# Kernel optimization log

Measured on AMD Instinct MI355X. Metric: run time of the kernel, lower is better.

The kernel has to match this reference:

```python
import jax, jax.numpy as jnp
import numpy as np

STRIDE = 1
PADDING = 1

def setup_inputs() -> dict:
    key = jax.random.key(0)
    k1, k2 = jax.random.split(key)
    x = jax.random.normal(k1, (16, 64, 224, 224), dtype=jnp.float32)
    weight = jax.random.normal(k2, (64, 64, 3, 3), dtype=jnp.float32)
    return {"x": x, "weight": weight}

def reference(x, weight):
    # Module's per-tap shift-and-add loop is exactly cross-correlation conv2d:
    # weight indexed [out, in, kh, kw] with ZeroPad2d(padding) and given stride.
    return jax.lax.conv_general_dilated(
        x, weight,
        window_strides=(STRIDE, STRIDE),
        padding=((PADDING, PADDING), (PADDING, PADDING)),
        dimension_numbers=("NCHW", "OIHW", "NCHW"),
    )
```

## Files before the change

### kernel.cpp

```cpp
#include <hip/hip_runtime.h>
#include <stdint.h>


#define HH 224
#define WW 224
#define CHW (HH * WW)
#define PLANE 4352
#define NSLOT 18
#define XT_ROWB 28928
#define XT_NB   6537728
#define WB_BYTES 73728
#define WS_NEED (WB_BYTES + 16 * (size_t)XT_NB)

typedef short bf16x8 __attribute__((ext_vector_type(8)));
typedef float f32x16 __attribute__((ext_vector_type(16)));
typedef __attribute__((address_space(1))) const char GCHAR;
typedef __attribute__((address_space(3))) char LCHAR;

__device__ __forceinline__ unsigned short f2bf(float f) {
    union { float f; unsigned int u; } v; v.f = f;
    unsigned int u = v.u;
    return (unsigned short)((u + 0x7fffu + ((u >> 16) & 1u)) >> 16);
}

#define SGB  __builtin_amdgcn_sched_group_barrier
#define MFMA __builtin_amdgcn_mfma_f32_32x32x16_bf16

__device__ __forceinline__ void block_fence_lds() {
    asm volatile("s_waitcnt lgkmcnt(0)" ::: "memory");
    __builtin_amdgcn_s_barrier();
    __builtin_amdgcn_sched_barrier(0);
}

__global__ void wprep_kernel(const float* __restrict__ wgt, unsigned short* __restrict__ wb) {
    const int i = blockIdx.x * 256 + threadIdx.x;
    if (i >= 36864) return;
    const int j   = i & 7;
    const int oc  = (i >> 3) & 63;
    const int g   = (i >> 9) & 1;
    const int ks  = i >> 10;
    const int tap = ks >> 2;
    const int c   = (ks & 3) * 16 + g * 8 + j;
    wb[i] = f2bf(wgt[(oc * 64 + c) * 9 + tap]);
}

__global__ __launch_bounds__(256)
void xprep_kernel(const float* __restrict__ x, unsigned short* __restrict__ xt) {
    __shared__ __align__(16) unsigned short tile[226 * 64];
    const int tid = threadIdx.x;
    const int b   = blockIdx.x;
    const int n   = b / 226;
    const int hp  = b % 226;
    bf16x8* orow = (bf16x8*)((char*)xt + (size_t)(n * 226 + hp) * XT_ROWB);

    if (hp == 0 || hp == 225) {
        const bf16x8 z = {};
        for (int i = tid; i < 1808; i += 256) orow[i] = z;
        return;
    }
    if (tid < 64) { tile[tid] = 0; tile[225 * 64 + tid] = 0; }

    const float* xr = x + (size_t)n * 64 * CHW + (size_t)(hp - 1) * WW;
    for (int i = tid; i < 64 * 56; i += 256) {
        const int c  = i / 56;
        const int w4 = i % 56;
        const float4 v = *(const float4*)(xr + (size_t)c * CHW + w4 * 4);
        const int wp0 = w4 * 4 + 1;
        const int cb  = c * 2;
        *(unsigned short*)((char*)tile + (wp0    ) * 128 + (cb ^ ((((wp0    ) >> 2) & 7) << 4))) = f2bf(v.x);
        *(unsigned short*)((char*)tile + (wp0 + 1) * 128 + (cb ^ ((((wp0 + 1) >> 2) & 7) << 4))) = f2bf(v.y);
        *(unsigned short*)((char*)tile + (wp0 + 2) * 128 + (cb ^ ((((wp0 + 2) >> 2) & 7) << 4))) = f2bf(v.z);
        *(unsigned short*)((char*)tile + (wp0 + 3) * 128 + (cb ^ ((((wp0 + 3) >> 2) & 7) << 4))) = f2bf(v.w);
    }
    __syncthreads();
    for (int i = tid; i < 1808; i += 256) {
        const int wp = i >> 3, k = i & 7;
        orow[i] = ((const bf16x8*)tile)[wp * 8 + (k ^ ((wp >> 2) & 7))];
    }
}

#define MMA_CQ(dw, cq, WFU) do {                                              \
    const int off_ = (((cq) * 32 + g16) ^ swz_);                              \
    const bf16x8 B0 = *(const bf16x8*)(ldsB + sl0 + wb_ + off_);              \
    const bf16x8 B1 = *(const bf16x8*)(ldsB + sl1 + wb_ + off_);              \
    const bf16x8 B2 = *(const bf16x8*)(ldsB + sl2 + wb_ + off_);              \
    const bf16x8 B3 = *(const bf16x8*)(ldsB + sl3 + wb_ + off_);              \
    const bf16x8 B4 = *(const bf16x8*)(ldsB + sl4 + wb_ + off_);              \
    const bf16x8 B5 = *(const bf16x8*)(ldsB + sl5 + wb_ + off_);              \
    a0 = MFMA(wfrag[(dw)*4 + (cq)], B0, a0, 0, 0, 0);                         \
    a1 = MFMA(wfrag[(dw)*4 + (cq)], B1, a1, 0, 0, 0);                         \
    a2 = MFMA(wfrag[(dw)*4 + (cq)], B2, a2, 0, 0, 0);                         \
    a3 = MFMA(wfrag[(dw)*4 + (cq)], B3, a3, 0, 0, 0);                         \
    a0 = MFMA(wfrag[12 + (dw)*4 + (cq)], B1, a0, 0, 0, 0);                    \
    a1 = MFMA(wfrag[12 + (dw)*4 + (cq)], B2, a1, 0, 0, 0);                    \
    a2 = MFMA(wfrag[12 + (dw)*4 + (cq)], B3, a2, 0, 0, 0);                    \
    a3 = MFMA(wfrag[12 + (dw)*4 + (cq)], B4, a3, 0, 0, 0);                    \
    a0 = MFMA(WFU, B2, a0, 0, 0, 0);                                          \
    a1 = MFMA(WFU, B3, a1, 0, 0, 0);                                          \
    a2 = MFMA(WFU, B4, a2, 0, 0, 0);                                          \
    a3 = MFMA(WFU, B5, a3, 0, 0, 0);                                          \
    SGB(0x100, 6, 0); SGB(0x008, 12, 0);                                      \
} while (0)

#define SECTION(dw, cqp, WFU0, WFU1, WFLD0, WFLD1, ldw, lcqp) do {            \
    WFLD0 = *(const bf16x8*)(wlane + ((6 + (ldw))*4 + 2*(lcqp)    ) * 1024);  \
    WFLD1 = *(const bf16x8*)(wlane + ((6 + (ldw))*4 + 2*(lcqp) + 1) * 1024);  \
    const int wl_  = s + (dw);                                                \
    const int swz_ = (wl_ & 7) << 4;                                          \
    const int wb_  = wl_ * 128;                                               \
    MMA_CQ(dw, 2*(cqp),     WFU0);                                            \
    MMA_CQ(dw, 2*(cqp) + 1, WFU1);                                            \
} while (0)

#define GLOAD_ROW(r) do {                                                     \
    const char* seg_ = xtn + (size_t)((r) + 1) * XT_ROWB;                     \
    char* lp_ = ldsB + (((r) + NSLOT) % NSLOT) * PLANE;                       \
    _Pragma("unroll")                                                         \
    for (int p_ = 0; p_ < 4; ++p_)                                            \
        __builtin_amdgcn_global_load_lds((GCHAR*)(seg_ + p_ * 1024 + lconst), \
                                         (LCHAR*)(lp_ + p_ * 1024), 16, 0, 0);\
    if (lane < 16)                                                            \
        __builtin_amdgcn_global_load_lds((GCHAR*)(seg_ + 4096 + lconst),      \
                                         (LCHAR*)(lp_ + 4096), 16, 0, 0);     \
} while (0)

__global__ __launch_bounds__(256, 2)
void conv3x3_gl(const unsigned short* __restrict__ xt, const unsigned short* __restrict__ wb,
                float* __restrict__ out) {
    __shared__ __align__(16) unsigned short lds[NSLOT * 34 * 64];
    char* ldsB = (char*)lds;

    const int tid  = threadIdx.x;
    const int lane = tid & 63;
    const int wv   = tid >> 6;
    const int och  = wv & 1;
    const int rg4  = wv >> 1;
    const int s    = lane & 31;
    const int g    = lane >> 5;
    const int g16  = g * 16;

    const int bid = blockIdx.x;
    const int n   = bid / 28;
    const int rem = bid % 28;
    const int ws  = rem / 4;
    const int hc  = rem % 4;
    const int wbase = ws * 32;
    const int h0    = hc * 56;

    const int lconst = ((lane >> 3) << 7) + (((lane & 7) ^ (lane >> 3)) << 4);
    const char* xtn = (const char*)xt + (size_t)n * XT_NB + (size_t)wbase * 128;

    const unsigned short* wlane = wb + g * 512 + (och * 32 + s) * 8;
    bf16x8 wfrag[24];
#pragma unroll
    for (int ks = 0; ks < 24; ++ks)
        wfrag[ks] = *(const bf16x8*)(wlane + ks * 1024);
    bf16x8 wfA0 = *(const bf16x8*)(wlane + 24 * 1024);
    bf16x8 wfA1 = *(const bf16x8*)(wlane + 25 * 1024);
    bf16x8 wfB0 = {}, wfB1 = {};

    for (int rr = 0; rr < 10; ++rr) {
        const int r = h0 - 1 + rr;
        const char* seg = xtn + (size_t)(r + 1) * XT_ROWB;
        char* lp = ldsB + ((r + NSLOT) % NSLOT) * PLANE;
        __builtin_amdgcn_global_load_lds((GCHAR*)(seg + wv * 1024 + lconst),
                                         (LCHAR*)(lp + wv * 1024), 16, 0, 0);
        if (wv == 0 && lane < 16)
            __builtin_amdgcn_global_load_lds((GCHAR*)(seg + 4096 + lconst),
                                             (LCHAR*)(lp + 4096), 16, 0, 0);
    }
    __syncthreads();

#pragma unroll 1
    for (int it = 0; it < 7; ++it) {
        const int h  = h0 + 8 * it;
        const int hb = h + 4 * rg4;

        if (it < 6) {
            const int r0 = h + 9 + 2 * wv;
            GLOAD_ROW(r0);
            GLOAD_ROW(r0 + 1);
        }

        int t_ = (hb - 1 + NSLOT) % NSLOT;
        const int sl0 = t_ * PLANE; t_ = (t_ + 1 == NSLOT) ? 0 : t_ + 1;
        const int sl1 = t_ * PLANE; t_ = (t_ + 1 == NSLOT) ? 0 : t_ + 1;
        const int sl2 = t_ * PLANE; t_ = (t_ + 1 == NSLOT) ? 0 : t_ + 1;
        const int sl3 = t_ * PLANE; t_ = (t_ + 1 == NSLOT) ? 0 : t_ + 1;
        const int sl4 = t_ * PLANE; t_ = (t_ + 1 == NSLOT) ? 0 : t_ + 1;
        const int sl5 = t_ * PLANE;

        f32x16 a0 = {}, a1 = {}, a2 = {}, a3 = {};

        SECTION(0, 0, wfA0, wfA1, wfB0, wfB1, 0, 1);
        SECTION(0, 1, wfB0, wfB1, wfA0, wfA1, 1, 0);
        SECTION(1, 0, wfA0, wfA1, wfB0, wfB1, 1, 1);
        SECTION(1, 1, wfB0, wfB1, wfA0, wfA1, 2, 0);
        SECTION(2, 0, wfA0, wfA1, wfB0, wfB1, 2, 1);
        SECTION(2, 1, wfB0, wfB1, wfA0, wfA1, 0, 0);

        float* po = out + (n * 64 + och * 32 + 4 * g) * CHW + hb * WW + wbase + s;
#pragma unroll
        for (int rg = 0; rg < 16; ++rg) {
            const int o_ = ((rg & 3) + 8 * (rg >> 2)) * CHW;
            po[o_]          = a0[rg];
            po[o_ + WW]     = a1[rg];
            po[o_ + 2 * WW] = a2[rg];
            po[o_ + 3 * WW] = a3[rg];
        }

        __syncthreads();
    }
}

#define STI(k) do { if (st) {                                                 \
    const int r_ = h + 9 + (k);                                               \
    const bool ok_ = (r_ < HH);                                               \
    _Pragma("unroll")                                                         \
    for (int j = 0; j < 8; ++j) pv[j] = ok_ ? pxm[j*CHW + r_*WW] : 0.f;       \
    if (tid >= 240) {                                                         \
        const bool okh_ = ok_ && hokw;                                        \
        _Pragma("unroll")                                                     \
        for (int j = 0; j < 8; ++j) hv[j] = okh_ ? pxh[j*CHW + r_*WW] : 0.f;  \
    } } } while (0)

#define STW(k) do { if (st) {                                                 \
    int sw_ = slw + (k); if (sw_ >= NSLOT) sw_ -= NSLOT;                      \
    bf16x8 f_;                                                                \
    _Pragma("unroll")                                                         \
    for (int j = 0; j < 8; ++j) f_[j] = (short)f2bf(pv[j]);                   \
    *(bf16x8*)(ldsB + sw_ * PLANE + lom) = f_;                                \
    if (tid >= 240) {                                                         \
        bf16x8 fh_;                                                           \
        _Pragma("unroll")                                                     \
        for (int j = 0; j < 8; ++j) fh_[j] = (short)f2bf(hv[j]);              \
        *(bf16x8*)(ldsB + sw_ * PLANE + loh) = fh_;                           \
    } } } while (0)

__global__ __launch_bounds__(256, 2)
void conv3x3_fb(const float* __restrict__ x, const unsigned short* __restrict__ wb,
                float* __restrict__ out) {
    __shared__ __align__(16) unsigned short lds[NSLOT * 34 * 64];
    char* ldsB = (char*)lds;

    const int tid  = threadIdx.x;
    const int lane = tid & 63;
    const int wv   = tid >> 6;
    const int och  = wv & 1;
    const int rg4  = wv >> 1;
    const int s    = lane & 31;
    const int g    = lane >> 5;
    const int g16  = g * 16;

    const int bid = blockIdx.x;
    const int n   = bid / 28;
    const int rem = bid % 28;
    const int ws  = rem / 4;
    const int hc  = rem % 4;
    const int wbase = ws * 32;
    const int h0    = hc * 56;

    const unsigned short* wlane = wb + g * 512 + (och * 32 + s) * 8;
    bf16x8 wfrag[24];
#pragma unroll
    for (int ks = 0; ks < 24; ++ks)
        wfrag[ks] = *(const bf16x8*)(wlane + ks * 1024);
    bf16x8 wfA0 = *(const bf16x8*)(wlane + 24 * 1024);
    bf16x8 wfA1 = *(const bf16x8*)(wlane + 25 * 1024);
    bf16x8 wfB0 = {}, wfB1 = {};

    for (int p = tid; p < 10 * 272; p += 256) {
        const int rrel = p / 272;
        const int q  = p % 272;
        const int c8 = q / 34;
        const int wl = q % 34;
        const int r  = h0 - 1 + rrel;
        const int gw = wbase - 1 + wl;
        bf16x8 f = {};
        if (r >= 0 && r < HH && gw >= 0 && gw < WW) {
            const float* px = x + (n * 64 + c8 * 8) * CHW + r * WW + gw;
#pragma unroll
            for (int j = 0; j < 8; ++j) f[j] = (short)f2bf(px[j * CHW]);
        }
        *(bf16x8*)(ldsB + ((r + NSLOT) % NSLOT) * PLANE + wl * 128
                   + ((c8 * 16) ^ ((wl & 7) << 4))) = f;
    }

    const int c8m = tid >> 5;
    const int wlm = 1 + (tid & 31);
    const float* pxm = x + (n * 64 + c8m * 8) * CHW + (wbase + (tid & 31));
    const int lom = wlm * 128 + ((c8m * 16) ^ ((wlm & 7) << 4));
    const int c8h = lane & 7;
    const int wlh = ((lane >> 3) & 1) * 33;
    const int gwh = wbase - 1 + wlh;
    const bool hokw = (gwh >= 0 && gwh < WW);
    const float* pxh = x + (n * 64 + c8h * 8) * CHW + gwh;
    const int loh = wlh * 128 + ((c8h * 16) ^ ((wlh & 7) << 4));

    block_fence_lds();

#pragma unroll 1
    for (int it = 0; it < 7; ++it) {
        const int h  = h0 + 8 * it;
        const int hb = h + 4 * rg4;
        const bool st = (it < 6);
        const int slw = (h + 9) % NSLOT;

        int t_ = (hb - 1 + NSLOT) % NSLOT;
        const int sl0 = t_ * PLANE; t_ = (t_ + 1 == NSLOT) ? 0 : t_ + 1;
        const int sl1 = t_ * PLANE; t_ = (t_ + 1 == NSLOT) ? 0 : t_ + 1;
        const int sl2 = t_ * PLANE; t_ = (t_ + 1 == NSLOT) ? 0 : t_ + 1;
        const int sl3 = t_ * PLANE; t_ = (t_ + 1 == NSLOT) ? 0 : t_ + 1;
        const int sl4 = t_ * PLANE; t_ = (t_ + 1 == NSLOT) ? 0 : t_ + 1;
        const int sl5 = t_ * PLANE;

        float pv[8], hv[8];
        f32x16 a0 = {}, a1 = {}, a2 = {}, a3 = {};

        STI(0); SECTION(0, 0, wfA0, wfA1, wfB0, wfB1, 0, 1); STW(0);
        STI(1); SECTION(0, 1, wfB0, wfB1, wfA0, wfA1, 1, 0); STW(1);
        STI(2); SECTION(1, 0, wfA0, wfA1, wfB0, wfB1, 1, 1); STW(2);
        STI(3); SECTION(1, 1, wfB0, wfB1, wfA0, wfA1, 2, 0); STW(3);
        STI(4); SECTION(2, 0, wfA0, wfA1, wfB0, wfB1, 2, 1); STW(4);
        STI(5); SECTION(2, 1, wfB0, wfB1, wfA0, wfA1, 0, 0); STW(5);

        float* po = out + (n * 64 + och * 32 + 4 * g) * CHW + hb * WW + wbase + s;
        STI(6);
#pragma unroll
        for (int rg = 0; rg < 16; ++rg) {
            const int o_ = ((rg & 3) + 8 * (rg >> 2)) * CHW;
            po[o_]      = a0[rg];
            po[o_ + WW] = a1[rg];
        }
        STW(6); STI(7);
#pragma unroll
        for (int rg = 0; rg < 16; ++rg) {
            const int o_ = ((rg & 3) + 8 * (rg >> 2)) * CHW;
            po[o_ + 2 * WW] = a2[rg];
            po[o_ + 3 * WW] = a3[rg];
        }
        STW(7);

        block_fence_lds();
    }
}

extern "C" void kernel_launch(void* const* d_in, const int* in_sizes, int n_in,
                              void* d_out, int out_size, void* d_ws, size_t ws_size,
                              hipStream_t stream) {
    const float* x   = (const float*)d_in[0];
    const float* wgt = (const float*)d_in[1];
    float* out       = (float*)d_out;
    unsigned short* wbuf = (unsigned short*)d_ws;

    wprep_kernel<<<dim3(144), dim3(256), 0, stream>>>(wgt, wbuf);
    if (ws_size >= WS_NEED) {
        unsigned short* xt = (unsigned short*)((char*)d_ws + WB_BYTES);
        xprep_kernel<<<dim3(16 * 226), dim3(256), 0, stream>>>(x, xt);
        conv3x3_gl<<<dim3(448), dim3(256), 0, stream>>>(xt, wbuf, out);
    } else {
        conv3x3_fb<<<dim3(448), dim3(256), 0, stream>>>(x, wbuf, out);
    }
}
```

Before: 161.6 us.

## Shrink conv tile to 2 rows per wave for higher occupancy and more blocks

Rewrites the main bf16 MFMA conv kernel so each wave computes 2 output rows instead of 4. The launch grows to 896 blocks of 28 rows each, and the LDS ring shrinks from 18 to 10 row slots. Only the first kw tap's weight fragments stay resident in registers; the other two taps' fragments stream from global memory each step. Launch bounds rise to 3 blocks per CU, aiming for better latency hiding and load balance across CUs. The costs are reloading the streamed weight fragments every iteration and reusing fewer input rows per LDS load.

```diff
diff --git a/kernel.cpp b/kernel.cpp
--- a/kernel.cpp
+++ b/kernel.cpp
@@ -7,6 +7,7 @@
 #define CHW (HH * WW)
 #define PLANE 4352
 #define NSLOT 18
+#define NSLOTG 10
 #define XT_ROWB 28928
 #define XT_NB   6537728
 #define WB_BYTES 73728
@@ -76,6 +77,112 @@
     for (int i = tid; i < 1808; i += 256) {
         const int wp = i >> 3, k = i & 7;
         orow[i] = ((const bf16x8*)tile)[wp * 8 + (k ^ ((wp >> 2) & 7))];
+    }
+}
+
+#define GLOAD_ROW(r) do {                                                     \
+    const char* seg_ = xtn + (size_t)((r) + 1) * XT_ROWB;                     \
+    char* lp_ = ldsB + (((r) + NSLOTG) % NSLOTG) * PLANE;                     \
+    _Pragma("unroll")                                                         \
+    for (int p_ = 0; p_ < 4; ++p_)                                            \
+        __builtin_amdgcn_global_load_lds((GCHAR*)(seg_ + p_ * 1024 + lconst), \
+                                         (LCHAR*)(lp_ + p_ * 1024), 16, 0, 0);\
+    if (lane < 16)                                                            \
+        __builtin_amdgcn_global_load_lds((GCHAR*)(seg_ + 4096 + lconst),      \
+                                         (LCHAR*)(lp_ + 4096), 16, 0, 0);     \
+} while (0)
+
+#define STEP(j, U1_, U2_) do {                                                \
+    const int wl_  = s + ((j) >> 2);                                          \
+    const int off_ = wl_ * 128 + ((((j) & 3) * 32 + g16) ^ ((wl_ & 7) << 4)); \
+    const bf16x8 B0 = *(const bf16x8*)(ldsB + sl0 + off_);                    \
+    const bf16x8 B1 = *(const bf16x8*)(ldsB + sl1 + off_);                    \
+    const bf16x8 B2 = *(const bf16x8*)(ldsB + sl2 + off_);                    \
+    const bf16x8 B3 = *(const bf16x8*)(ldsB + sl3 + off_);                    \
+    a0 = MFMA(wfrag[(j)], B0, a0, 0, 0, 0);                                   \
+    a1 = MFMA(wfrag[(j)], B1, a1, 0, 0, 0);                                   \
+    a0 = MFMA(U1_, B1, a0, 0, 0, 0);                                          \
+    a1 = MFMA(U1_, B2, a1, 0, 0, 0);                                          \
+    a0 = MFMA(U2_, B2, a0, 0, 0, 0);                                          \
+    a1 = MFMA(U2_, B3, a1, 0, 0, 0);                                          \
+    SGB(0x100, 4, 0); SGB(0x008, 6, 0);                                       \
+    U1_ = *(const bf16x8*)(wlane + (12 + ((j) + 4) % 12) * 1024);             \
+    U2_ = *(const bf16x8*)(wlane + (24 + ((j) + 4) % 12) * 1024);             \
+} while (0)
+
+__global__ __launch_bounds__(256, 3)
+void conv3x3_gl(const unsigned short* __restrict__ xt, const unsigned short* __restrict__ wb,
+                float* __restrict__ out) {
+    __shared__ __align__(16) unsigned short lds[NSLOTG * 34 * 64];
+    char* ldsB = (char*)lds;
+
+    const int tid  = threadIdx.x;
+    const int lane = tid & 63;
+    const int wv   = tid >> 6;
+    const int och  = wv & 1;
+    const int rp   = wv >> 1;
+    const int s    = lane & 31;
+    const int g    = lane >> 5;
+    const int g16  = g * 16;
+
+    const int bid = blockIdx.x;
+    const int n   = bid / 56;
+    const int rem = bid % 56;
+    const int ws  = rem / 8;
+    const int hc  = rem % 8;
+    const int wbase = ws * 32;
+    const int h0    = hc * 28;
+
+    const int lconst = ((lane >> 3) << 7) + (((lane & 7) ^ (lane >> 3)) << 4);
+    const char* xtn = (const char*)xt + (size_t)n * XT_NB + (size_t)wbase * 128;
+
+    const unsigned short* wlane = wb + g * 512 + (och * 32 + s) * 8;
+    bf16x8 wfrag[12];
+#pragma unroll
+    for (int ks = 0; ks < 12; ++ks)
+        wfrag[ks] = *(const bf16x8*)(wlane + ks * 1024);
+    bf16x8 Q1a = *(const bf16x8*)(wlane + 12 * 1024);
+    bf16x8 Q1b = *(const bf16x8*)(wlane + 13 * 1024);
+    bf16x8 Q1c = *(const bf16x8*)(wlane + 14 * 1024);
+    bf16x8 Q1d = *(const bf16x8*)(wlane + 15 * 1024);
+    bf16x8 Q2a = *(const bf16x8*)(wlane + 24 * 1024);
+    bf16x8 Q2b = *(const bf16x8*)(wlane + 25 * 1024);
+    bf16x8 Q2c = *(const bf16x8*)(wlane + 26 * 1024);
+    bf16x8 Q2d = *(const bf16x8*)(wlane + 27 * 1024);
+
+    for (int rr = wv; rr < 6; rr += 4) {
+        const int r = h0 - 1 + rr;
+        GLOAD_ROW(r);
+    }
+    __syncthreads();
+
+#pragma unroll 1
+    for (int it = 0; it < 7; ++it) {
+        const int h  = h0 + 4 * it;
+        const int hb = h + 2 * rp;
+
+        if (it < 6) GLOAD_ROW(h + 5 + wv);
+
+        const int sl0 = ((hb - 1 + 2 * NSLOTG) % NSLOTG) * PLANE;
+        const int sl1 = ((hb     + 2 * NSLOTG) % NSLOTG) * PLANE;
+        const int sl2 = ((hb + 1) % NSLOTG) * PLANE;
+        const int sl3 = ((hb + 2) % NSLOTG) * PLANE;
+
+        f32x16 a0 = {}, a1 = {};
+
+        STEP(0, Q1a, Q2a); STEP(1, Q1b, Q2b); STEP(2, Q1c, Q2c); STEP(3, Q1d, Q2d);
+        STEP(4, Q1a, Q2a); STEP(5, Q1b, Q2b); STEP(6, Q1c, Q2c); STEP(7, Q1d, Q2d);
+        STEP(8, Q1a, Q2a); STEP(9, Q1b, Q2b); STEP(10, Q1c, Q2c); STEP(11, Q1d, Q2d);
+
+        float* po = out + (n * 64 + och * 32 + 4 * g) * CHW + hb * WW + wbase + s;
+#pragma unroll
+        for (int rg = 0; rg < 16; ++rg) {
+            const int o_ = ((rg & 3) + 8 * (rg >> 2)) * CHW;
+            po[o_]      = a0[rg];
+            po[o_ + WW] = a1[rg];
+        }
+
+        __syncthreads();
     }
 }
 
@@ -112,107 +219,6 @@
     MMA_CQ(dw, 2*(cqp) + 1, WFU1);                                            \
 } while (0)
 
-#define GLOAD_ROW(r) do {                                                     \
-    const char* seg_ = xtn + (size_t)((r) + 1) * XT_ROWB;                     \
-    char* lp_ = ldsB + (((r) + NSLOT) % NSLOT) * PLANE;                       \
-    _Pragma("unroll")                                                         \
-    for (int p_ = 0; p_ < 4; ++p_)                                            \
-        __builtin_amdgcn_global_load_lds((GCHAR*)(seg_ + p_ * 1024 + lconst), \
-                                         (LCHAR*)(lp_ + p_ * 1024), 16, 0, 0);\
-    if (lane < 16)                                                            \
-        __builtin_amdgcn_global_load_lds((GCHAR*)(seg_ + 4096 + lconst),      \
-                                         (LCHAR*)(lp_ + 4096), 16, 0, 0);     \
-} while (0)
-
-__global__ __launch_bounds__(256, 2)
-void conv3x3_gl(const unsigned short* __restrict__ xt, const unsigned short* __restrict__ wb,
-                float* __restrict__ out) {
-    __shared__ __align__(16) unsigned short lds[NSLOT * 34 * 64];
-    char* ldsB = (char*)lds;
-
-    const int tid  = threadIdx.x;
-    const int lane = tid & 63;
-    const int wv   = tid >> 6;
-    const int och  = wv & 1;
-    const int rg4  = wv >> 1;
-    const int s    = lane & 31;
-    const int g    = lane >> 5;
-    const int g16  = g * 16;
-
-    const int bid = blockIdx.x;
-    const int n   = bid / 28;
-    const int rem = bid % 28;
-    const int ws  = rem / 4;
-    const int hc  = rem % 4;
-    const int wbase = ws * 32;
-    const int h0    = hc * 56;
-
-    const int lconst = ((lane >> 3) << 7) + (((lane & 7) ^ (lane >> 3)) << 4);
-    const char* xtn = (const char*)xt + (size_t)n * XT_NB + (size_t)wbase * 128;
-
-    const unsigned short* wlane = wb + g * 512 + (och * 32 + s) * 8;
-    bf16x8 wfrag[24];
-#pragma unroll
-    for (int ks = 0; ks < 24; ++ks)
-        wfrag[ks] = *(const bf16x8*)(wlane + ks * 1024);
-    bf16x8 wfA0 = *(const bf16x8*)(wlane + 24 * 1024);
-    bf16x8 wfA1 = *(const bf16x8*)(wlane + 25 * 1024);
-    bf16x8 wfB0 = {}, wfB1 = {};
-
-    for (int rr = 0; rr < 10; ++rr) {
-        const int r = h0 - 1 + rr;
-        const char* seg = xtn + (size_t)(r + 1) * XT_ROWB;
-        char* lp = ldsB + ((r + NSLOT) % NSLOT) * PLANE;
-        __builtin_amdgcn_global_load_lds((GCHAR*)(seg + wv * 1024 + lconst),
-                                         (LCHAR*)(lp + wv * 1024), 16, 0, 0);
-        if (wv == 0 && lane < 16)
-            __builtin_amdgcn_global_load_lds((GCHAR*)(seg + 4096 + lconst),
-                                             (LCHAR*)(lp + 4096), 16, 0, 0);
-    }
-    __syncthreads();
-
-#pragma unroll 1
-    for (int it = 0; it < 7; ++it) {
-        const int h  = h0 + 8 * it;
-        const int hb = h + 4 * rg4;
-
-        if (it < 6) {
-            const int r0 = h + 9 + 2 * wv;
-            GLOAD_ROW(r0);
-            GLOAD_ROW(r0 + 1);
-        }
-
-        int t_ = (hb - 1 + NSLOT) % NSLOT;
-        const int sl0 = t_ * PLANE; t_ = (t_ + 1 == NSLOT) ? 0 : t_ + 1;
-        const int sl1 = t_ * PLANE; t_ = (t_ + 1 == NSLOT) ? 0 : t_ + 1;
-        const int sl2 = t_ * PLANE; t_ = (t_ + 1 == NSLOT) ? 0 : t_ + 1;
-        const int sl3 = t_ * PLANE; t_ = (t_ + 1 == NSLOT) ? 0 : t_ + 1;
-        const int sl4 = t_ * PLANE; t_ = (t_ + 1 == NSLOT) ? 0 : t_ + 1;
-        const int sl5 = t_ * PLANE;
-
-        f32x16 a0 = {}, a1 = {}, a2 = {}, a3 = {};
-
-        SECTION(0, 0, wfA0, wfA1, wfB0, wfB1, 0, 1);
-        SECTION(0, 1, wfB0, wfB1, wfA0, wfA1, 1, 0);
-        SECTION(1, 0, wfA0, wfA1, wfB0, wfB1, 1, 1);
-        SECTION(1, 1, wfB0, wfB1, wfA0, wfA1, 2, 0);
-        SECTION(2, 0, wfA0, wfA1, wfB0, wfB1, 2, 1);
-        SECTION(2, 1, wfB0, wfB1, wfA0, wfA1, 0, 0);
-
-        float* po = out + (n * 64 + och * 32 + 4 * g) * CHW + hb * WW + wbase + s;
-#pragma unroll
-        for (int rg = 0; rg < 16; ++rg) {
-            const int o_ = ((rg & 3) + 8 * (rg >> 2)) * CHW;
-            po[o_]          = a0[rg];
-            po[o_ + WW]     = a1[rg];
-            po[o_ + 2 * WW] = a2[rg];
-            po[o_ + 3 * WW] = a3[rg];
-        }
-
-        __syncthreads();
-    }
-}
-
 #define STI(k) do { if (st) {                                                 \
     const int r_ = h + 9 + (k);                                               \
     const bool ok_ = (r_ < HH);                                               \
@@ -357,7 +363,7 @@
     if (ws_size >= WS_NEED) {
         unsigned short* xt = (unsigned short*)((char*)d_ws + WB_BYTES);
         xprep_kernel<<<dim3(16 * 226), dim3(256), 0, stream>>>(x, xt);
-        conv3x3_gl<<<dim3(448), dim3(256), 0, stream>>>(xt, wbuf, out);
+        conv3x3_gl<<<dim3(16 * 7 * 8), dim3(256), 0, stream>>>(xt, wbuf, out);
     } else {
         conv3x3_fb<<<dim3(448), dim3(256), 0, stream>>>(x, wbuf, out);
     }
```

After: 211.1 us. 1.31x slower.

## Retile width to 28 columns so grid has 512 blocks filling all CUs

Applied to the files above, without the earlier changes.

Changes the fast-path conv kernel tiling from 32-wide to 28-wide column strips. This gives 8 strips per image and a grid of 512 blocks instead of 448, which should spread the work more evenly over the 256 CUs with 2 blocks each and avoid a partial second wave. The LDS plane shrinks to 30 columns (plus padding), and loads are adjusted to match. Each MFMA still computes 32 columns, so 4 of 32 lanes' outputs are discarded (about 12.5% wasted compute). The fallback kernel keeps the old plane size through separate macros.

```diff
diff --git a/kernel.cpp b/kernel.cpp
--- a/kernel.cpp
+++ b/kernel.cpp
@@ -5,7 +5,7 @@
 #define HH 224
 #define WW 224
 #define CHW (HH * WW)
-#define PLANE 4352
+#define PLANE 3840
 #define NSLOT 18
 #define XT_ROWB 28928
 #define XT_NB   6537728
@@ -116,18 +116,18 @@
     const char* seg_ = xtn + (size_t)((r) + 1) * XT_ROWB;                     \
     char* lp_ = ldsB + (((r) + NSLOT) % NSLOT) * PLANE;                       \
     _Pragma("unroll")                                                         \
-    for (int p_ = 0; p_ < 4; ++p_)                                            \
+    for (int p_ = 0; p_ < 3; ++p_)                                            \
         __builtin_amdgcn_global_load_lds((GCHAR*)(seg_ + p_ * 1024 + lconst), \
                                          (LCHAR*)(lp_ + p_ * 1024), 16, 0, 0);\
-    if (lane < 16)                                                            \
-        __builtin_amdgcn_global_load_lds((GCHAR*)(seg_ + 4096 + lconst),      \
-                                         (LCHAR*)(lp_ + 4096), 16, 0, 0);     \
+    if (lane < 48)                                                            \
+        __builtin_amdgcn_global_load_lds((GCHAR*)(seg_ + 3072 + lconst),      \
+                                         (LCHAR*)(lp_ + 3072), 16, 0, 0);     \
 } while (0)
 
 __global__ __launch_bounds__(256, 2)
 void conv3x3_gl(const unsigned short* __restrict__ xt, const unsigned short* __restrict__ wb,
                 float* __restrict__ out) {
-    __shared__ __align__(16) unsigned short lds[NSLOT * 34 * 64];
+    __shared__ __align__(16) unsigned short lds[NSLOT * 30 * 64 + 256];
     char* ldsB = (char*)lds;
 
     const int tid  = threadIdx.x;
@@ -140,11 +140,11 @@
     const int g16  = g * 16;
 
     const int bid = blockIdx.x;
-    const int n   = bid / 28;
-    const int rem = bid % 28;
+    const int n   = bid / 32;
+    const int rem = bid % 32;
     const int ws  = rem / 4;
     const int hc  = rem % 4;
-    const int wbase = ws * 32;
+    const int wbase = ws * 28;
     const int h0    = hc * 56;
 
     const int lconst = ((lane >> 3) << 7) + (((lane & 7) ^ (lane >> 3)) << 4);
@@ -163,11 +163,9 @@
         const int r = h0 - 1 + rr;
         const char* seg = xtn + (size_t)(r + 1) * XT_ROWB;
         char* lp = ldsB + ((r + NSLOT) % NSLOT) * PLANE;
-        __builtin_amdgcn_global_load_lds((GCHAR*)(seg + wv * 1024 + lconst),
-                                         (LCHAR*)(lp + wv * 1024), 16, 0, 0);
-        if (wv == 0 && lane < 16)
-            __builtin_amdgcn_global_load_lds((GCHAR*)(seg + 4096 + lconst),
-                                             (LCHAR*)(lp + 4096), 16, 0, 0);
+        if (wv < 3 || lane < 48)
+            __builtin_amdgcn_global_load_lds((GCHAR*)(seg + wv * 1024 + lconst),
+                                             (LCHAR*)(lp + wv * 1024), 16, 0, 0);
     }
     __syncthreads();
 
@@ -199,20 +197,23 @@
         SECTION(2, 0, wfA0, wfA1, wfB0, wfB1, 2, 1);
         SECTION(2, 1, wfB0, wfB1, wfA0, wfA1, 0, 0);
 
-        float* po = out + (n * 64 + och * 32 + 4 * g) * CHW + hb * WW + wbase + s;
-#pragma unroll
-        for (int rg = 0; rg < 16; ++rg) {
-            const int o_ = ((rg & 3) + 8 * (rg >> 2)) * CHW;
-            po[o_]          = a0[rg];
-            po[o_ + WW]     = a1[rg];
-            po[o_ + 2 * WW] = a2[rg];
-            po[o_ + 3 * WW] = a3[rg];
+        if (s < 28) {
+            float* po = out + (n * 64 + och * 32 + 4 * g) * CHW + hb * WW + wbase + s;
+#pragma unroll
+            for (int rg = 0; rg < 16; ++rg) {
+                const int o_ = ((rg & 3) + 8 * (rg >> 2)) * CHW;
+                po[o_]          = a0[rg];
+                po[o_ + WW]     = a1[rg];
+                po[o_ + 2 * WW] = a2[rg];
+                po[o_ + 3 * WW] = a3[rg];
+            }
         }
 
         __syncthreads();
     }
 }
 
+#define PLANE_FB 4352
 #define STI(k) do { if (st) {                                                 \
     const int r_ = h + 9 + (k);                                               \
     const bool ok_ = (r_ < HH);                                               \
@@ -229,13 +230,46 @@
     bf16x8 f_;                                                                \
     _Pragma("unroll")                                                         \
     for (int j = 0; j < 8; ++j) f_[j] = (short)f2bf(pv[j]);                   \
-    *(bf16x8*)(ldsB + sw_ * PLANE + lom) = f_;                                \
+    *(bf16x8*)(ldsB + sw_ * PLANE_FB + lom) = f_;                             \
     if (tid >= 240) {                                                         \
         bf16x8 fh_;                                                           \
         _Pragma("unroll")                                                     \
         for (int j = 0; j < 8; ++j) fh_[j] = (short)f2bf(hv[j]);              \
-        *(bf16x8*)(ldsB + sw_ * PLANE + loh) = fh_;                           \
+        *(bf16x8*)(ldsB + sw_ * PLANE_FB + loh) = fh_;                        \
     } } } while (0)
+
+#define MMA_CQ_FB(dw, cq, WFU) do {                                           \
+    const int off_ = (((cq) * 32 + g16) ^ swz_);                              \
+    const bf16x8 B0 = *(const bf16x8*)(ldsB + sl0 + wb_ + off_);              \
+    const bf16x8 B1 = *(const bf16x8*)(ldsB + sl1 + wb_ + off_);              \
+    const bf16x8 B2 = *(const bf16x8*)(ldsB + sl2 + wb_ + off_);              \
+    const bf16x8 B3 = *(const bf16x8*)(ldsB + sl3 + wb_ + off_);              \
+    const bf16x8 B4 = *(const bf16x8*)(ldsB + sl4 + wb_ + off_);              \
+    const bf16x8 B5 = *(const bf16x8*)(ldsB + sl5 + wb_ + off_);              \
+    a0 = MFMA(wfrag[(dw)*4 + (cq)], B0, a0, 0, 0, 0);                         \
+    a1 = MFMA(wfrag[(dw)*4 + (cq)], B1, a1, 0, 0, 0);                         \
+    a2 = MFMA(wfrag[(dw)*4 + (cq)], B2, a2, 0, 0, 0);                         \
+    a3 = MFMA(wfrag[(dw)*4 + (cq)], B3, a3, 0, 0, 0);                         \
+    a0 = MFMA(wfrag[12 + (dw)*4 + (cq)], B1, a0, 0, 0, 0);                    \
+    a1 = MFMA(wfrag[12 + (dw)*4 + (cq)], B2, a1, 0, 0, 0);                    \
+    a2 = MFMA(wfrag[12 + (dw)*4 + (cq)], B3, a2, 0, 0, 0);                    \
+    a3 = MFMA(wfrag[12 + (dw)*4 + (cq)], B4, a3, 0, 0, 0);                    \
+    a0 = MFMA(WFU, B2, a0, 0, 0, 0);                                          \
+    a1 = MFMA(WFU, B3, a1, 0, 0, 0);                                          \
+    a2 = MFMA(WFU, B4, a2, 0, 0, 0);                                          \
+    a3 = MFMA(WFU, B5, a3, 0, 0, 0);                                          \
+    SGB(0x100, 6, 0); SGB(0x008, 12, 0);                                      \
+} while (0)
+
+#define SECTION_FB(dw, cqp, WFU0, WFU1, WFLD0, WFLD1, ldw, lcqp) do {         \
+    WFLD0 = *(const bf16x8*)(wlane + ((6 + (ldw))*4 + 2*(lcqp)    ) * 1024);  \
+    WFLD1 = *(const bf16x8*)(wlane + ((6 + (ldw))*4 + 2*(lcqp) + 1) * 1024);  \
+    const int wl_  = s + (dw);                                                \
+    const int swz_ = (wl_ & 7) << 4;                                          \
+    const int wb_  = wl_ * 128;                                               \
+    MMA_CQ_FB(dw, 2*(cqp),     WFU0);                                         \
+    MMA_CQ_FB(dw, 2*(cqp) + 1, WFU1);                                         \
+} while (0)
 
 __global__ __launch_bounds__(256, 2)
 void conv3x3_fb(const float* __restrict__ x, const unsigned short* __restrict__ wb,
@@ -282,7 +316,7 @@
 #pragma unroll
             for (int j = 0; j < 8; ++j) f[j] = (short)f2bf(px[j * CHW]);
         }
-        *(bf16x8*)(ldsB + ((r + NSLOT) % NSLOT) * PLANE + wl * 128
+        *(bf16x8*)(ldsB + ((r + NSLOT) % NSLOT) * PLANE_FB + wl * 128
                    + ((c8 * 16) ^ ((wl & 7) << 4))) = f;
     }
 
@@ -307,22 +341,22 @@
         const int slw = (h + 9) % NSLOT;
 
         int t_ = (hb - 1 + NSLOT) % NSLOT;
-        const int sl0 = t_ * PLANE; t_ = (t_ + 1 == NSLOT) ? 0 : t_ + 1;
-        const int sl1 = t_ * PLANE; t_ = (t_ + 1 == NSLOT) ? 0 : t_ + 1;
-        const int sl2 = t_ * PLANE; t_ = (t_ + 1 == NSLOT) ? 0 : t_ + 1;
-        const int sl3 = t_ * PLANE; t_ = (t_ + 1 == NSLOT) ? 0 : t_ + 1;
-        const int sl4 = t_ * PLANE; t_ = (t_ + 1 == NSLOT) ? 0 : t_ + 1;
-        const int sl5 = t_ * PLANE;
+        const int sl0 = t_ * PLANE_FB; t_ = (t_ + 1 == NSLOT) ? 0 : t_ + 1;
+        const int sl1 = t_ * PLANE_FB; t_ = (t_ + 1 == NSLOT) ? 0 : t_ + 1;
+        const int sl2 = t_ * PLANE_FB; t_ = (t_ + 1 == NSLOT) ? 0 : t_ + 1;
+        const int sl3 = t_ * PLANE_FB; t_ = (t_ + 1 == NSLOT) ? 0 : t_ + 1;
+        const int sl4 = t_ * PLANE_FB; t_ = (t_ + 1 == NSLOT) ? 0 : t_ + 1;
+        const int sl5 = t_ * PLANE_FB;
 
         float pv[8], hv[8];
         f32x16 a0 = {}, a1 = {}, a2 = {}, a3 = {};
 
-        STI(0); SECTION(0, 0, wfA0, wfA1, wfB0, wfB1, 0, 1); STW(0);
-        STI(1); SECTION(0, 1, wfB0, wfB1, wfA0, wfA1, 1, 0); STW(1);
-        STI(2); SECTION(1, 0, wfA0, wfA1, wfB0, wfB1, 1, 1); STW(2);
-        STI(3); SECTION(1, 1, wfB0, wfB1, wfA0, wfA1, 2, 0); STW(3);
-        STI(4); SECTION(2, 0, wfA0, wfA1, wfB0, wfB1, 2, 1); STW(4);
-        STI(5); SECTION(2, 1, wfB0, wfB1, wfA0, wfA1, 0, 0); STW(5);
+        STI(0); SECTION_FB(0, 0, wfA0, wfA1, wfB0, wfB1, 0, 1); STW(0);
+        STI(1); SECTION_FB(0, 1, wfB0, wfB1, wfA0, wfA1, 1, 0); STW(1);
+        STI(2); SECTION_FB(1, 0, wfA0, wfA1, wfB0, wfB1, 1, 1); STW(2);
+        STI(3); SECTION_FB(1, 1, wfB0, wfB1, wfA0, wfA1, 2, 0); STW(3);
+        STI(4); SECTION_FB(2, 0, wfA0, wfA1, wfB0, wfB1, 2, 1); STW(4);
+        STI(5); SECTION_FB(2, 1, wfB0, wfB1, wfA0, wfA1, 0, 0); STW(5);
 
         float* po = out + (n * 64 + och * 32 + 4 * g) * CHW + hb * WW + wbase + s;
         STI(6);
@@ -357,7 +391,7 @@
     if (ws_size >= WS_NEED) {
         unsigned short* xt = (unsigned short*)((char*)d_ws + WB_BYTES);
         xprep_kernel<<<dim3(16 * 226), dim3(256), 0, stream>>>(x, xt);
-        conv3x3_gl<<<dim3(448), dim3(256), 0, stream>>>(xt, wbuf, out);
+        conv3x3_gl<<<dim3(512), dim3(256), 0, stream>>>(xt, wbuf, out);
     } else {
         conv3x3_fb<<<dim3(448), dim3(256), 0, stream>>>(x, wbuf, out);
     }
```

Measured after the change: 205.1 us. +26.9%, slower.
